# Kernel optimization log

Hardware: AMD Instinct MI355X
Metric: run time of the kernel (lower is better)

The kernel has to match this reference:

```python
import jax, jax.numpy as jnp
import numpy as np

N, E, B = 8192, 131072, 256
F_ATOM, D, H, HD, L, FC, BINS = 92, 256, 8, 32, 6, 512, 256
VMIN, VMAX = 0.0, 8.0


def layer_norm(x, g, b, eps=1e-5):
    mu = jnp.mean(x, axis=-1, keepdims=True)
    var = jnp.var(x, axis=-1, keepdims=True)
    return (x - mu) * jax.lax.rsqrt(var + eps) * g + b


def silu(x):
    return x * jax.nn.sigmoid(x)


def setup_inputs() -> dict:
    key = jax.random.key(0)
    ks = iter(jax.random.split(key, 80))

    def lin(fan_in, shape):
        return jax.random.normal(next(ks), shape, jnp.float32) / np.sqrt(fan_in)

    inp = {
        'x': jax.random.normal(next(ks), (N, F_ATOM), jnp.float32),
        'edge_attr': jax.random.normal(next(ks), (E, 3), jnp.float32) * 2.0,
        'edge_index': jax.random.randint(next(ks), (2, E), 0, N, dtype=jnp.int32),
        'batch': jnp.sort(jax.random.randint(next(ks), (N,), 0, B, dtype=jnp.int32)),
        # atom_embedding: Linear(92,256) -> LN -> SiLU -> Linear(256,256)
        'aw1': lin(F_ATOM, (F_ATOM, D)), 'ab1': jnp.zeros((D,)),
        'ag1': jnp.ones((D,)), 'abt1': jnp.zeros((D,)),
        'aw2': lin(D, (D, D)), 'ab2': jnp.zeros((D,)),
        # rbf MLP: Linear(256,256) LN SiLU Linear LN SiLU Linear
        'rw1': lin(BINS, (BINS, D)), 'rb1': jnp.zeros((D,)),
        'rg1': jnp.ones((D,)), 'rbt1': jnp.zeros((D,)),
        'rw2': lin(D, (D, D)), 'rb2': jnp.zeros((D,)),
        'rg2': jnp.ones((D,)), 'rbt2': jnp.zeros((D,)),
        'rw3': lin(D, (D, D)), 'rb3': jnp.zeros((D,)),
        # L stacked PrdnetConv (edge-conditioned multi-head graph attention)
        'Wq': lin(D, (L, D, D)), 'bq': jnp.zeros((L, D)),
        'Wk': lin(D, (L, D, D)), 'bk': jnp.zeros((L, D)),
        'Wv': lin(D, (L, D, D)), 'bv': jnp.zeros((L, D)),
        'We': lin(D, (L, D, D)), 'be': jnp.zeros((L, D)),
        'Wo': lin(D, (L, D, D)), 'bo': jnp.zeros((L, D)),
        'lng': jnp.ones((L, D)), 'lnb': jnp.zeros((L, D)),
        # FC head: Linear(256,512) then fc_out Linear(512,1)
        'fw1': lin(D, (D, FC)), 'fb1': jnp.zeros((FC,)),
        'fow': lin(FC, (FC, 1)), 'fob': jnp.zeros((1,)),
    }
    return inp


def _forward(x, edge_attr, edge_index, batch, aw1, ab1, ag1, abt1, aw2, ab2,
             rw1, rb1, rg1, rbt1, rw2, rb2, rg2, rbt2, rw3, rb3,
             Wq, bq, Wk, bk, Wv, bv, We, be, Wo, bo, lng, lnb,
             fw1, fb1, fow, fob):
    # atom embedding (dropout = identity at inference)
    node = silu(layer_norm(x @ aw1 + ab1, ag1, abt1)) @ aw2 + ab2  # [N, D]

    # RBF expansion of edge lengths, then edge MLP
    d = jnp.linalg.norm(edge_attr, axis=1)  # [E]
    centers = jnp.linspace(VMIN, VMAX, BINS)
    gamma = 1.0 / (centers[1] - centers[0]) ** 2
    rbf = jnp.exp(-gamma * (d[:, None] - centers[None, :]) ** 2)  # [E, BINS]
    e = silu(layer_norm(rbf @ rw1 + rb1, rg1, rbt1))
    e = silu(layer_norm(e @ rw2 + rb2, rg2, rbt2))
    e = e @ rw3 + rb3  # [E, D]

    src, dst = edge_index[0], edge_index[1]
    inv_sqrt = 1.0 / np.sqrt(HD)
    for l in range(L):
        res = node
        q = (node @ Wq[l] + bq[l]).reshape(N, H, HD)
        k = (node @ Wk[l] + bk[l]).reshape(N, H, HD)
        v = (node @ Wv[l] + bv[l]).reshape(N, H, HD)
        ee = (e @ We[l] + be[l]).reshape(E, H, HD)
        kj = k[src] + ee  # edge-conditioned keys [E, H, HD]
        vj = v[src] + ee  # edge-conditioned values
        score = jnp.sum(q[dst] * kj, axis=-1) * inv_sqrt  # [E, H]
        smax = jax.ops.segment_max(score, dst, num_segments=N)  # [N, H]
        ex = jnp.exp(score - smax[dst])
        den = jax.ops.segment_sum(ex, dst, num_segments=N)
        alpha = ex / (den[dst] + 1e-16)  # neighborhood softmax [E, H]
        msg = jax.ops.segment_sum(alpha[:, :, None] * vj, dst, num_segments=N)
        out = msg.reshape(N, D) @ Wo[l] + bo[l]
        out = layer_norm(out, lng[l], lnb[l])
        node = out + res  # residual

    # scatter-mean graph pooling
    sums = jax.ops.segment_sum(node, batch, num_segments=B)  # [B, D]
    cnt = jax.ops.segment_sum(jnp.ones((N,), node.dtype), batch, num_segments=B)
    feats = sums / jnp.clip(cnt, 1.0)[:, None]

    feats = feats @ fw1 + fb1  # single fc layer: no act (i == len-1 in source)
    return feats @ fow + fob  # [B, 1], identity link


def reference(x, edge_attr, edge_index, batch, aw1, ab1, ag1, abt1, aw2, ab2,
              rw1, rb1, rg1, rbt1, rw2, rb2, rg2, rbt2, rw3, rb3,
              Wq, bq, Wk, bk, Wv, bv, We, be, Wo, bo, lng, lnb,
              fw1, fb1, fow, fob):
    return _forward(x, edge_attr, edge_index, batch, aw1, ab1, ag1, abt1, aw2,
                    ab2, rw1, rb1, rg1, rbt1, rw2, rb2, rg2, rbt2, rw3, rb3,
                    Wq, bq, Wk, bk, Wv, bv, We, be, Wo, bo, lng, lnb,
                    fw1, fb1, fow, fob)
```

## Files before the change

kernel.cpp:

```cpp
#include <hip/hip_runtime.h>
#include <hip/hip_bf16.h>
#include <cstddef>

#define NN    8192
#define EE    131072
#define BB    256
#define F_AT  92
#define DD    256
#define HH    8
#define HDIM  32
#define LL    6
#define FCD   512

typedef __hip_bfloat16 bf16;
typedef __attribute__((ext_vector_type(8))) __bf16 bf16x8;
typedef __attribute__((ext_vector_type(4))) float f32x4;

__device__ __forceinline__ float to_f(float x) { return x; }
__device__ __forceinline__ float to_f(bf16 x) { return __bfloat162float(x); }
__device__ __forceinline__ float bfu(unsigned short u) {
    return __uint_as_float(((unsigned)u) << 16);
}
__device__ __forceinline__ unsigned short bfbits(float x) {
    bf16 h = __float2bfloat16(x);
    return *(unsigned short*)&h;
}
__device__ __forceinline__ void store_v(float* p, float v) { *p = v; }
__device__ __forceinline__ void store_v(bf16* p, float v) { *p = __float2bfloat16(v); }

__device__ __forceinline__ float4 load4(const float* p) { return *(const float4*)p; }
__device__ __forceinline__ float4 load4(const bf16* p) {
    const ushort4 r = *(const ushort4*)p;
    return make_float4(bfu(r.x), bfu(r.y), bfu(r.z), bfu(r.w));
}

__device__ __forceinline__ void store_f4(float* p, const float4& f) {
    *(float4*)p = f;
}
__device__ __forceinline__ void store_f4(bf16* p, const float4& f) {
    ushort4 u = {bfbits(f.x), bfbits(f.y), bfbits(f.z), bfbits(f.w)};
    *(ushort4*)p = u;
}

__device__ __forceinline__ bf16x8 ld8(const bf16* p) { return *(const bf16x8*)p; }
__device__ __forceinline__ bf16x8 ld8(const float* p) {
    const float4 f0 = *(const float4*)p;
    const float4 f1 = *(const float4*)(p + 4);
    bf16x8 r;
    r[0] = (__bf16)f0.x; r[1] = (__bf16)f0.y; r[2] = (__bf16)f0.z; r[3] = (__bf16)f0.w;
    r[4] = (__bf16)f1.x; r[5] = (__bf16)f1.y; r[6] = (__bf16)f1.z; r[7] = (__bf16)f1.w;
    return r;
}

__device__ __forceinline__ void async_copy16(const void* g, void* l) {
    __builtin_amdgcn_global_load_lds(
        (const __attribute__((address_space(1))) unsigned int*)g,
        (__attribute__((address_space(3))) unsigned int*)l, 16, 0, 0);
}

__global__ __launch_bounds__(256) void transpose_weights(
    const float* __restrict__ rw1, const float* __restrict__ rw2,
    const float* __restrict__ rw3, const float* __restrict__ aw2,
    const float* __restrict__ Wq, const float* __restrict__ Wk,
    const float* __restrict__ Wv, const float* __restrict__ We,
    const float* __restrict__ Wo, __bf16* __restrict__ out)
{
    __shared__ float tile[64][65];
    const int midx = blockIdx.y;
    const float* src;
    if (midx == 0) src = rw1;
    else if (midx == 1) src = rw2;
    else if (midx == 2) src = rw3;
    else if (midx == 3) src = aw2;
    else {
        const int l = (midx - 4) / 5, s = (midx - 4) % 5;
        const float* bases[5] = {Wq, Wk, Wv, We, Wo};
        src = bases[s] + (size_t)l * 65536;
    }
    __bf16* dst = out + (size_t)midx * 65536;
    const int k0 = (blockIdx.x >> 2) * 64;
    const int n0 = (blockIdx.x & 3) * 64;
    const int c = threadIdx.x & 63;
    const int r0 = threadIdx.x >> 6;
#pragma unroll
    for (int p = 0; p < 16; ++p) {
        const int r = r0 + p * 4;
        tile[r][c] = src[(size_t)(k0 + r) * 256 + n0 + c];
    }
    __syncthreads();
#pragma unroll
    for (int p = 0; p < 16; ++p) {
        const int n = r0 + p * 4;
        dst[(size_t)(n0 + n) * 256 + k0 + c] = (__bf16)tile[c][n];
    }
}

__global__ __launch_bounds__(256) void pack_qkv_bias(
    const float* __restrict__ bq, const float* __restrict__ bk,
    const float* __restrict__ bv, float* __restrict__ out)
{
    const int i = blockIdx.x * 256 + threadIdx.x;
    if (i >= LL * 768) return;
    const int l = i / 768, r = i % 768;
    const float* s = (r < 256) ? bq : (r < 512) ? bk : bv;
    out[i] = s[l * 256 + (r & 255)];
}

__global__ __launch_bounds__(256) void combine_w3e(
    const float* __restrict__ rw3, const float* __restrict__ We,
    __bf16* __restrict__ Wt_out)
{
    __shared__ float As[16][65];
    __shared__ float Ws[16][65];
    const int l = blockIdx.z;
    const float* W = We + (size_t)l * 65536;
    __bf16* dst = Wt_out + (size_t)l * 65536;
    const int m0 = blockIdx.x * 64;
    const int n0 = blockIdx.y * 64;
    const int tid = threadIdx.x;
    const int tx = tid & 15, ty = tid >> 4;
    float acc[4][4] = {};

    for (int k0 = 0; k0 < 256; k0 += 16) {
        {
            const int ar = tid >> 2;
            const int ac = (tid & 3) * 4;
#pragma unroll
            for (int j = 0; j < 4; ++j)
                As[ac + j][ar] = rw3[(size_t)(m0 + ar) * 256 + k0 + ac + j];
        }
        {
            const int wr = tid >> 4;
            const int wc = (tid & 15) * 4;
#pragma unroll
            for (int j = 0; j < 4; ++j)
                Ws[wr][wc + j] = W[(size_t)(k0 + wr) * 256 + n0 + wc + j];
        }
        __syncthreads();
#pragma unroll
        for (int kk = 0; kk < 16; ++kk) {
            float a[4], b[4];
#pragma unroll
            for (int i = 0; i < 4; ++i) a[i] = As[kk][ty * 4 + i];
#pragma unroll
            for (int j = 0; j < 4; ++j) b[j] = Ws[kk][tx * 4 + j];
#pragma unroll
            for (int i = 0; i < 4; ++i)
#pragma unroll
                for (int j = 0; j < 4; ++j) acc[i][j] += a[i] * b[j];
        }
        __syncthreads();
    }
#pragma unroll
    for (int i = 0; i < 4; ++i) {
        const int gk = m0 + ty * 4 + i;
#pragma unroll
        for (int j = 0; j < 4; ++j) {
            const int gn = n0 + tx * 4 + j;
            dst[(size_t)gn * 256 + gk] = (__bf16)acc[i][j];
        }
    }
}

__global__ __launch_bounds__(256) void combine_bias(
    const float* __restrict__ rb3, const float* __restrict__ We,
    const float* __restrict__ be, float* __restrict__ out)
{
    const int l = blockIdx.x;
    const int n = threadIdx.x;
    const float* W = We + (size_t)l * 65536;
    float s = be[l * 256 + n];
    for (int m = 0; m < 256; ++m) s += rb3[m] * W[m * 256 + n];
    out[l * 256 + n] = s;
}

__global__ __launch_bounds__(256) void mfma_gemm_ln(
    const bf16* __restrict__ A, const __bf16* __restrict__ Wt,
    const float* __restrict__ bias, const float* __restrict__ g,
    const float* __restrict__ b, bf16* __restrict__ C, int do_silu)
{
    __shared__ __align__(16) __bf16 As[64 * 64];
    __shared__ __align__(16) __bf16 Bs[256 * 64];
    const int tid = threadIdx.x;
    const int m0 = blockIdx.x * 64;
    const int wave = tid >> 6, lane = tid & 63;
    const int lm = lane & 15, lq = lane >> 4;
    const int lrow = lane >> 3;
    const int lcolsw = ((lane & 7) ^ lrow) * 8;

    f32x4 acc[16] = {};

    for (int k0 = 0; k0 < 256; k0 += 64) {
#pragma unroll
        for (int p = 0; p < 2; ++p) {
            const int rbase = wave * 16 + p * 8;
            async_copy16(A + (size_t)(m0 + rbase + lrow) * 256 + k0 + lcolsw,
                         As + rbase * 64);
        }
#pragma unroll
        for (int p = 0; p < 8; ++p) {
            const int rbase = wave * 64 + p * 8;
            async_copy16(Wt + (size_t)(rbase + lrow) * 256 + k0 + lcolsw,
                         Bs + rbase * 64);
        }
        __syncthreads();
#pragma unroll
        for (int ks = 0; ks < 2; ++ks) {
            const int sw = ((ks * 4 + lq) ^ (lm & 7)) * 8;
            const bf16x8 a = *(const bf16x8*)(As + (wave * 16 + lm) * 64 + sw);
#pragma unroll
            for (int j = 0; j < 16; ++j) {
                const bf16x8 bf = *(const bf16x8*)(Bs + (j * 16 + lm) * 64 + sw);
                acc[j] = __builtin_amdgcn_mfma_f32_16x16x32_bf16(a, bf, acc[j], 0, 0, 0);
            }
        }
        __syncthreads();
    }

    float gg[16], bb[16];
#pragma unroll
    for (int j = 0; j < 16; ++j) {
        const float bv = bias[j * 16 + lm];
        gg[j] = g[j * 16 + lm];
        bb[j] = b[j * 16 + lm];
#pragma unroll
        for (int r = 0; r < 4; ++r) acc[j][r] += bv;
    }

#pragma unroll
    for (int r = 0; r < 4; ++r) {
        float s = 0.f, q = 0.f;
#pragma unroll
        for (int j = 0; j < 16; ++j) { const float v = acc[j][r]; s += v; q += v * v; }
#pragma unroll
        for (int msk = 1; msk < 16; msk <<= 1) {
            s += __shfl_xor(s, msk);
            q += __shfl_xor(q, msk);
        }
        const float mean = s * (1.f / 256.f);
        const float var = q * (1.f / 256.f) - mean * mean;
        const float rs = rsqrtf(var + 1e-5f);
        bf16* crow = C + (size_t)(m0 + wave * 16 + lq * 4 + r) * 256;
#pragma unroll
        for (int j = 0; j < 16; ++j) {
            float v = (acc[j][r] - mean) * rs * gg[j] + bb[j];
            if (do_silu) v = v / (1.f + __expf(-v));
            crow[j * 16 + lm] = __float2bfloat16(v);
        }
    }
}

template <typename CT>
__global__ __launch_bounds__(256) void mfma_gemm_async(
    const bf16* __restrict__ A, const __bf16* __restrict__ Wt,
    const float* __restrict__ bias, CT* __restrict__ C,
    int M, int Nn, int K)
{
    __shared__ __align__(16) __bf16 As[128 * 64];
    __shared__ __align__(16) __bf16 Bs[128 * 64];
    const int tid = threadIdx.x;
    const int m0 = blockIdx.x * 128;
    const int n0 = blockIdx.y * 128;
    const int wave = tid >> 6, lane = tid & 63;
    const int wm = (wave & 1) * 64, wn = (wave >> 1) * 64;
    const int lm = lane & 15, lq = lane >> 4;
    const int lrow = lane >> 3;
    const int lcolsw = ((lane & 7) ^ lrow) * 8;

    f32x4 acc[4][4] = {};

    for (int k0 = 0; k0 < K; k0 += 64) {
#pragma unroll
        for (int p = 0; p < 4; ++p) {
            const int rbase = wave * 32 + p * 8;
            async_copy16(A  + (size_t)(m0 + rbase + lrow) * K + k0 + lcolsw,
                         As + rbase * 64);
            async_copy16(Wt + (size_t)(n0 + rbase + lrow) * K + k0 + lcolsw,
                         Bs + rbase * 64);
        }
        __syncthreads();
#pragma unroll
        for (int ks = 0; ks < 2; ++ks) {
            const int sw = ((ks * 4 + lq) ^ (lm & 7)) * 8;
            bf16x8 a[4], b[4];
#pragma unroll
            for (int i = 0; i < 4; ++i) {
                a[i] = *(const bf16x8*)(As + (wm + i * 16 + lm) * 64 + sw);
                b[i] = *(const bf16x8*)(Bs + (wn + i * 16 + lm) * 64 + sw);
            }
#pragma unroll
            for (int i = 0; i < 4; ++i)
#pragma unroll
                for (int j = 0; j < 4; ++j)
                    acc[i][j] = __builtin_amdgcn_mfma_f32_16x16x32_bf16(
                        a[i], b[j], acc[i][j], 0, 0, 0);
        }
        __syncthreads();
    }

#pragma unroll
    for (int i = 0; i < 4; ++i) {
        const int gm = m0 + wm + i * 16 + lq * 4;
#pragma unroll
        for (int j = 0; j < 4; ++j) {
            const int gn = n0 + wn + j * 16 + lm;
            const float bv = bias ? bias[gn] : 0.f;
#pragma unroll
            for (int r = 0; r < 4; ++r)
                store_v(&C[(size_t)(gm + r) * Nn + gn], acc[i][j][r] + bv);
        }
    }
}

template <typename AT, typename CT>
__global__ __launch_bounds__(256) void mfma_gemm(
    const AT* __restrict__ A, const __bf16* __restrict__ Wt,
    const float* __restrict__ bias, CT* __restrict__ C,
    int M, int Nn, int K)
{
    __shared__ __align__(16) __bf16 As[128 * 72];
    __shared__ __align__(16) __bf16 Bs[128 * 72];
    const int tid = threadIdx.x;
    const int m0 = blockIdx.x * 128;
    const int n0 = blockIdx.y * 128;
    const int wave = tid >> 6, lane = tid & 63;
    const int wm = (wave & 1) * 64, wn = (wave >> 1) * 64;
    const int lm = lane & 15, lq = lane >> 4;

    f32x4 acc[4][4] = {};

    const int srow = tid >> 3;
    const int scol = (tid & 7) * 8;

    for (int k0 = 0; k0 < K; k0 += 64) {
#pragma unroll
        for (int p = 0; p < 4; ++p) {
            const int r = srow + 32 * p;
            *(bf16x8*)(As + r * 72 + scol) = ld8(A + (size_t)(m0 + r) * K + k0 + scol);
            *(bf16x8*)(Bs + r * 72 + scol) = *(const bf16x8*)(Wt + (size_t)(n0 + r) * K + k0 + scol);
        }
        __syncthreads();
#pragma unroll
        for (int ks = 0; ks < 2; ++ks) {
            bf16x8 a[4], b[4];
#pragma unroll
            for (int i = 0; i < 4; ++i) {
                a[i] = *(const bf16x8*)(As + (wm + i * 16 + lm) * 72 + ks * 32 + lq * 8);
                b[i] = *(const bf16x8*)(Bs + (wn + i * 16 + lm) * 72 + ks * 32 + lq * 8);
            }
#pragma unroll
            for (int i = 0; i < 4; ++i)
#pragma unroll
                for (int j = 0; j < 4; ++j)
                    acc[i][j] = __builtin_amdgcn_mfma_f32_16x16x32_bf16(
                        a[i], b[j], acc[i][j], 0, 0, 0);
        }
        __syncthreads();
    }

#pragma unroll
    for (int i = 0; i < 4; ++i) {
        const int gm = m0 + wm + i * 16 + lq * 4;
#pragma unroll
        for (int j = 0; j < 4; ++j) {
            const int gn = n0 + wn + j * 16 + lm;
            const float bv = bias ? bias[gn] : 0.f;
#pragma unroll
            for (int r = 0; r < 4; ++r)
                store_v(&C[(size_t)(gm + r) * Nn + gn], acc[i][j][r] + bv);
        }
    }
}

template <typename AT, typename CT>
__global__ __launch_bounds__(256) void gemm_bias(
    const AT* __restrict__ A, const float* __restrict__ W,
    const float* __restrict__ bias, CT* __restrict__ C,
    int M, int Nn, int K)
{
    __shared__ float As[16][65];
    __shared__ float Ws[16][65];
    const int m0 = blockIdx.x * 64;
    const int n0 = blockIdx.y * 64;
    const int tid = threadIdx.x;
    const int tx = tid & 15, ty = tid >> 4;
    float acc[4][4] = {};

    for (int k0 = 0; k0 < K; k0 += 16) {
        {
            const int ar = tid >> 2;
            const int ac = (tid & 3) * 4;
            const int gm = m0 + ar;
#pragma unroll
            for (int j = 0; j < 4; ++j) {
                const int gk = k0 + ac + j;
                float v = 0.f;
                if (gm < M && gk < K) v = to_f(A[(size_t)gm * K + gk]);
                As[ac + j][ar] = v;
            }
        }
        {
            const int wr = tid >> 4;
            const int wc = (tid & 15) * 4;
            const int gk = k0 + wr;
#pragma unroll
            for (int j = 0; j < 4; ++j) {
                float v = 0.f;
                if (gk < K) v = W[(size_t)gk * Nn + n0 + wc + j];
                Ws[wr][wc + j] = v;
            }
        }
        __syncthreads();
#pragma unroll
        for (int kk = 0; kk < 16; ++kk) {
            float a[4], b[4];
#pragma unroll
            for (int i = 0; i < 4; ++i) a[i] = As[kk][ty * 4 + i];
#pragma unroll
            for (int j = 0; j < 4; ++j) b[j] = Ws[kk][tx * 4 + j];
#pragma unroll
            for (int i = 0; i < 4; ++i)
#pragma unroll
                for (int j = 0; j < 4; ++j) acc[i][j] += a[i] * b[j];
        }
        __syncthreads();
    }
#pragma unroll
    for (int i = 0; i < 4; ++i) {
        const int gm = m0 + ty * 4 + i;
        if (gm >= M) continue;
#pragma unroll
        for (int j = 0; j < 4; ++j) {
            const int gn = n0 + tx * 4 + j;
            float v = acc[i][j];
            if (bias) v += bias[gn];
            store_v(&C[(size_t)gm * Nn + gn], v);
        }
    }
}

__global__ __launch_bounds__(256) void rbf_kernel(
    const float* __restrict__ ea, bf16* __restrict__ rbf)
{
    const int e = blockIdx.x * 4 + (threadIdx.x >> 6);
    const int c0 = (threadIdx.x & 63) * 4;
    const float ax = ea[e * 3 + 0];
    const float ay = ea[e * 3 + 1];
    const float az = ea[e * 3 + 2];
    const float d = sqrtf(ax * ax + ay * ay + az * az);
    const float step = 8.0f / 255.0f;
    const float gamma = 1.0f / (step * step);
    float o[4];
#pragma unroll
    for (int j = 0; j < 4; ++j) {
        const float t = d - (float)(c0 + j) * step;
        o[j] = __expf(-gamma * t * t);
    }
    store_f4(rbf + (size_t)e * DD + c0, make_float4(o[0], o[1], o[2], o[3]));
}

template <typename XT, typename YT>
__global__ __launch_bounds__(256) void ln_act_kernel(
    const XT* __restrict__ X, YT* __restrict__ Y,
    const float* __restrict__ g, const float* __restrict__ b,
    const float* __restrict__ resid, int rows, int do_silu)
{
    const int wave = threadIdx.x >> 6;
    const int lane = threadIdx.x & 63;
    const int r = blockIdx.x * 4 + wave;
    if (r >= rows) return;
    const float4 x = load4(X + (size_t)r * DD + lane * 4);
    float s = x.x + x.y + x.z + x.w;
    float q = x.x * x.x + x.y * x.y + x.z * x.z + x.w * x.w;
    for (int off = 32; off; off >>= 1) {
        s += __shfl_down(s, off);
        q += __shfl_down(q, off);
    }
    s = __shfl(s, 0);
    q = __shfl(q, 0);
    const float mean = s * (1.f / 256.f);
    const float var = q * (1.f / 256.f) - mean * mean;
    const float rs = rsqrtf(var + 1e-5f);
    const int c = lane * 4;
    float xs[4] = {x.x, x.y, x.z, x.w};
    float out[4];
#pragma unroll
    for (int i = 0; i < 4; ++i) {
        float v = (xs[i] - mean) * rs * g[c + i] + b[c + i];
        if (do_silu) v = v / (1.f + __expf(-v));
        out[i] = v;
    }
    if (resid) {
        const float4 rv = load4(resid + (size_t)r * DD + c);
        out[0] += rv.x; out[1] += rv.y; out[2] += rv.z; out[3] += rv.w;
    }
    store_f4(Y + (size_t)r * DD + c, make_float4(out[0], out[1], out[2], out[3]));
}

__global__ __launch_bounds__(256) void deg_kernel(
    const int* __restrict__ dst, int* __restrict__ deg)
{
    const int e = blockIdx.x * 256 + threadIdx.x;
    if (e < EE) atomicAdd(&deg[dst[e]], 1);
}

__global__ __launch_bounds__(256) void csr_scan(
    const int* __restrict__ deg, int* __restrict__ rowptr)
{
    __shared__ int part[256];
    const int t = threadIdx.x;
    int local[32];
    int s = 0;
#pragma unroll
    for (int i = 0; i < 32; ++i) { local[i] = deg[t * 32 + i]; s += local[i]; }
    part[t] = s;
    __syncthreads();
    if (t == 0) {
        int run = 0;
        for (int i = 0; i < 256; ++i) { const int v = part[i]; part[i] = run; run += v; }
    }
    __syncthreads();
    int run = part[t];
#pragma unroll
    for (int i = 0; i < 32; ++i) { rowptr[t * 32 + i] = run; run += local[i]; }
    if (t == 255) rowptr[NN] = run;
}

__global__ __launch_bounds__(256) void fill_kernel(
    const int* __restrict__ dst, const int* __restrict__ rowptr,
    int* __restrict__ fill, int* __restrict__ eid)
{
    const int e = blockIdx.x * 256 + threadIdx.x;
    if (e >= EE) return;
    const int d = dst[e];
    const int pos = atomicAdd(&fill[d], 1);
    eid[rowptr[d] + pos] = e;
}

__global__ __launch_bounds__(256) void attn_kernel(
    const bf16* __restrict__ qkv, const bf16* __restrict__ ee,
    const int* __restrict__ rowptr, const int* __restrict__ eid,
    const int* __restrict__ src, float* __restrict__ msg)
{
    const int n = blockIdx.x;
    const int tid = threadIdx.x;
    const int wave = tid >> 6, lane = tid & 63;
    const int e0 = rowptr[n];
    const int deg = rowptr[n + 1] - e0;

    if (deg == 0) {
        msg[(size_t)n * DD + tid] = 0.f;
        return;
    }

    __shared__ float wm[4][HH];
    __shared__ float wl[4][HH];
    __shared__ float wacc[4][DD];

    const float4 qreg = load4(qkv + (size_t)n * 768 + lane * 4);

    float m = -3.402823466e38f, l = 0.f;
    float4 acc = {0.f, 0.f, 0.f, 0.f};

    for (int j = wave; j < deg; j += 4) {
        const int e = eid[e0 + j];
        const int s_ = src[e];
        const bf16* srow = qkv + (size_t)s_ * 768;
        const float4 kv = load4(srow + 256 + lane * 4);
        const float4 vv = load4(srow + 512 + lane * 4);
        const float4 ev = load4(ee + (size_t)e * DD + lane * 4);
        float p = qreg.x * (kv.x + ev.x) + qreg.y * (kv.y + ev.y) +
                  qreg.z * (kv.z + ev.z) + qreg.w * (kv.w + ev.w);
        p += __shfl_down(p, 4);
        p += __shfl_down(p, 2);
        p += __shfl_down(p, 1);
        const float s = __shfl(p, lane & 56) * 0.17677669529663687f;
        const float mnew = fmaxf(m, s);
        const float scale = __expf(m - mnew);
        const float pe = __expf(s - mnew);
        l = l * scale + pe;
        acc.x = acc.x * scale + pe * (vv.x + ev.x);
        acc.y = acc.y * scale + pe * (vv.y + ev.y);
        acc.z = acc.z * scale + pe * (vv.z + ev.z);
        acc.w = acc.w * scale + pe * (vv.w + ev.w);
        m = mnew;
    }

    if ((lane & 7) == 0) { wm[wave][lane >> 3] = m; wl[wave][lane >> 3] = l; }
    *(float4*)(&wacc[wave][lane * 4]) = acc;
    __syncthreads();

    {
        const int c = tid, h = tid >> 5;
        float M = wm[0][h];
#pragma unroll
        for (int i = 1; i < 4; ++i) M = fmaxf(M, wm[i][h]);
        float L = 0.f, num = 0.f;
#pragma unroll
        for (int i = 0; i < 4; ++i) {
            const float sc = __expf(wm[i][h] - M);
            L += wl[i][h] * sc;
            num += wacc[i][c] * sc;
        }
        msg[(size_t)n * DD + c] = num / (L + 1e-16f);
    }
}

__global__ __launch_bounds__(256) void zero_kernel(float* __restrict__ p, int n)
{
    const int i = blockIdx.x * 256 + threadIdx.x;
    if (i < n) p[i] = 0.f;
}

__global__ __launch_bounds__(256) void pool_kernel(
    const float* __restrict__ node, const int* __restrict__ batch,
    float* __restrict__ sums, float* __restrict__ cnt)
{
    const int n = blockIdx.x;
    const int c = threadIdx.x;
    const int b = batch[n];
    atomicAdd(&sums[b * DD + c], node[(size_t)n * DD + c]);
    if (c == 0) atomicAdd(&cnt[b], 1.0f);
}

__global__ __launch_bounds__(256) void pooled_kernel(
    const float* __restrict__ sums, const float* __restrict__ cnt,
    float* __restrict__ pooled)
{
    const int b = blockIdx.x;
    const int c = threadIdx.x;
    float cc = cnt[b];
    if (cc < 1.f) cc = 1.f;
    pooled[b * DD + c] = sums[b * DD + c] / cc;
}

__global__ __launch_bounds__(64) void final_kernel(
    const float* __restrict__ fc, const float* __restrict__ fow,
    const float* __restrict__ fob, float* __restrict__ out)
{
    const int b = blockIdx.x;
    const int lane = threadIdx.x;
    float s = 0.f;
#pragma unroll
    for (int i = lane; i < FCD; i += 64) s += fc[(size_t)b * FCD + i] * fow[i];
    for (int off = 32; off; off >>= 1) s += __shfl_down(s, off);
    if (lane == 0) out[b] = s + fob[0];
}

extern "C" void kernel_launch(void* const* d_in, const int* in_sizes, int n_in,
                              void* d_out, int out_size, void* d_ws,
                              size_t ws_size, hipStream_t stream)
{
    const float* x         = (const float*)d_in[0];
    const float* edge_attr = (const float*)d_in[1];
    const int*   eidx      = (const int*)d_in[2];
    const int*   batch     = (const int*)d_in[3];
    const float* aw1 = (const float*)d_in[4];
    const float* ab1 = (const float*)d_in[5];
    const float* ag1 = (const float*)d_in[6];
    const float* abt1 = (const float*)d_in[7];
    const float* aw2 = (const float*)d_in[8];
    const float* ab2 = (const float*)d_in[9];
    const float* rw1 = (const float*)d_in[10];
    const float* rb1 = (const float*)d_in[11];
    const float* rg1 = (const float*)d_in[12];
    const float* rbt1 = (const float*)d_in[13];
    const float* rw2 = (const float*)d_in[14];
    const float* rb2 = (const float*)d_in[15];
    const float* rg2 = (const float*)d_in[16];
    const float* rbt2 = (const float*)d_in[17];
    const float* rw3 = (const float*)d_in[18];
    const float* rb3 = (const float*)d_in[19];
    const float* Wq = (const float*)d_in[20];
    const float* bq = (const float*)d_in[21];
    const float* Wk = (const float*)d_in[22];
    const float* bk = (const float*)d_in[23];
    const float* Wv = (const float*)d_in[24];
    const float* bv = (const float*)d_in[25];
    const float* We_ = (const float*)d_in[26];
    const float* be_ = (const float*)d_in[27];
    const float* Wo = (const float*)d_in[28];
    const float* bo = (const float*)d_in[29];
    const float* lng = (const float*)d_in[30];
    const float* lnb = (const float*)d_in[31];
    const float* fw1 = (const float*)d_in[32];
    const float* fb1 = (const float*)d_in[33];
    const float* fow = (const float*)d_in[34];
    const float* fob = (const float*)d_in[35];

    const int* src = eidx;
    const int* dst = eidx + EE;

    char* w = (char*)d_ws;
    size_t off = 0;
    auto alloc = [&](size_t bytes) -> void* {
        void* p = w + off;
        off += (bytes + 255) & ~(size_t)255;
        return p;
    };
    bf16* t_buf = (bf16*)alloc((size_t)EE * DD * 2);
    bf16* e_buf = (bf16*)alloc((size_t)EE * DD * 2);
    float* node = (float*)alloc((size_t)NN * DD * 4);
    bf16*  qkv  = (bf16*)alloc((size_t)NN * 768 * 2);
    float* msg  = (float*)alloc((size_t)NN * DD * 4);
    float* outb = (float*)alloc((size_t)NN * DD * 4);
    int* deg    = (int*)alloc((size_t)NN * 4);
    int* fillc  = (int*)alloc((size_t)NN * 4);
    int* rowptr = (int*)alloc((size_t)(NN + 1) * 4);
    int* eid    = (int*)alloc((size_t)EE * 4);
    float* sums  = (float*)alloc((size_t)BB * DD * 4);
    float* cnt   = (float*)alloc((size_t)BB * 4);
    float* pooled = (float*)alloc((size_t)BB * DD * 4);
    float* fc    = (float*)alloc((size_t)BB * FCD * 4);
    __bf16* Wt  = (__bf16*)alloc((size_t)40 * 65536 * 2);
    float* qkvb = (float*)alloc((size_t)LL * 768 * 4);
    float* be_c = (float*)alloc((size_t)LL * 256 * 4);
    (void)ws_size; (void)n_in; (void)in_sizes; (void)out_size;

    const dim3 blk(256);
    auto WT = [&](int i) -> const __bf16* { return Wt + (size_t)i * 65536; };

    hipLaunchKernelGGL(transpose_weights, dim3(16, 34), blk, 0, stream,
                       rw1, rw2, rw3, aw2, Wq, Wk, Wv, We_, Wo, Wt);
    hipLaunchKernelGGL(combine_w3e, dim3(4, 4, LL), blk, 0, stream, rw3, We_, Wt + (size_t)34 * 65536);
    hipLaunchKernelGGL(combine_bias, dim3(LL), blk, 0, stream, rb3, We_, be_, be_c);
    hipLaunchKernelGGL(pack_qkv_bias, dim3((LL * 768 + 255) / 256), blk, 0, stream, bq, bk, bv, qkvb);
    hipLaunchKernelGGL(zero_kernel, dim3((2 * NN + 255) / 256), blk, 0, stream, (float*)deg, 2 * NN);
    hipLaunchKernelGGL(deg_kernel, dim3(EE / 256), blk, 0, stream, dst, deg);
    hipLaunchKernelGGL(csr_scan, dim3(1), blk, 0, stream, deg, rowptr);
    hipLaunchKernelGGL(fill_kernel, dim3(EE / 256), blk, 0, stream, dst, rowptr, fillc, eid);

    hipLaunchKernelGGL(rbf_kernel, dim3(EE / 4), blk, 0, stream, edge_attr, t_buf);
    hipLaunchKernelGGL(mfma_gemm_ln, dim3(EE / 64), blk, 0, stream, t_buf, WT(0), rb1, rg1, rbt1, e_buf, 1);
    hipLaunchKernelGGL(mfma_gemm_ln, dim3(EE / 64), blk, 0, stream, e_buf, WT(1), rb2, rg2, rbt2, t_buf, 1);

    {
        dim3 gn64(NN / 64, DD / 64);
        hipLaunchKernelGGL((gemm_bias<float, float>), gn64, blk, 0, stream, x, aw1, ab1, outb, NN, DD, F_AT);
        hipLaunchKernelGGL((ln_act_kernel<float, float>), dim3(NN / 4), blk, 0, stream, outb, outb, ag1, abt1, (const float*)nullptr, NN, 1);
        hipLaunchKernelGGL((mfma_gemm<float, float>), dim3(NN / 128, DD / 128), blk, 0, stream, outb, WT(3), ab2, node, NN, DD, DD);
    }

    const dim3 geM(EE / 128, DD / 128);
    for (int l = 0; l < LL; ++l) {
        const size_t bo_ = (size_t)l * DD;
        hipLaunchKernelGGL((mfma_gemm<float, bf16>), dim3(NN / 128, 768 / 128), blk, 0, stream,
                           node, WT(4 + 5 * l), qkvb + (size_t)l * 768, qkv, NN, 768, DD);
        hipLaunchKernelGGL((mfma_gemm_async<bf16>), geM, blk, 0, stream, t_buf, WT(34 + l), be_c + (size_t)l * 256, e_buf, EE, DD, DD);
        hipLaunchKernelGGL(attn_kernel, dim3(NN), blk, 0, stream, qkv, e_buf, rowptr, eid, src, msg);
        hipLaunchKernelGGL((mfma_gemm<float, float>), dim3(NN / 128, DD / 128), blk, 0, stream, msg, WT(8 + 5 * l), bo + bo_, outb, NN, DD, DD);
        hipLaunchKernelGGL((ln_act_kernel<float, float>), dim3(NN / 4), blk, 0, stream, outb, node, lng + bo_, lnb + bo_, node, NN, 0);
    }

    const int PZ = BB * DD + BB;
    hipLaunchKernelGGL(zero_kernel, dim3((PZ + 255) / 256), blk, 0, stream, sums, PZ);
    hipLaunchKernelGGL(pool_kernel, dim3(NN), blk, 0, stream, node, batch, sums, cnt);
    hipLaunchKernelGGL(pooled_kernel, dim3(BB), blk, 0, stream, sums, cnt, pooled);
    {
        dim3 gf(BB / 64, FCD / 64);
        hipLaunchKernelGGL((gemm_bias<float, float>), gf, blk, 0, stream, pooled, fw1, fb1, fc, BB, FCD, DD);
    }
    hipLaunchKernelGGL(final_kernel, dim3(BB), dim3(64), 0, stream, fc, fow, fob, (float*)d_out);
}
```

Baseline: 1.043 ms.

## Reorder edge features into CSR order and batch edge projections across layers

```diff
diff --git a/kernel.cpp b/kernel.cpp
--- a/kernel.cpp
+++ b/kernel.cpp
@@ -440,9 +440,11 @@
 }
 
 __global__ __launch_bounds__(256) void rbf_kernel(
-    const float* __restrict__ ea, bf16* __restrict__ rbf)
-{
-    const int e = blockIdx.x * 4 + (threadIdx.x >> 6);
+    const float* __restrict__ ea, const int* __restrict__ eid,
+    bf16* __restrict__ rbf)
+{
+    const int p = blockIdx.x * 4 + (threadIdx.x >> 6);
+    const int e = eid[p];
     const int c0 = (threadIdx.x & 63) * 4;
     const float ax = ea[e * 3 + 0];
     const float ay = ea[e * 3 + 1];
@@ -456,7 +458,7 @@
         const float t = d - (float)(c0 + j) * step;
         o[j] = __expf(-gamma * t * t);
     }
-    store_f4(rbf + (size_t)e * DD + c0, make_float4(o[0], o[1], o[2], o[3]));
+    store_f4(rbf + (size_t)p * DD + c0, make_float4(o[0], o[1], o[2], o[3]));
 }
 
 template <typename XT, typename YT>
@@ -527,20 +529,23 @@
 }
 
 __global__ __launch_bounds__(256) void fill_kernel(
-    const int* __restrict__ dst, const int* __restrict__ rowptr,
-    int* __restrict__ fill, int* __restrict__ eid)
+    const int* __restrict__ src, const int* __restrict__ dst,
+    const int* __restrict__ rowptr, int* __restrict__ fill,
+    int* __restrict__ eid, int* __restrict__ srcc)
 {
     const int e = blockIdx.x * 256 + threadIdx.x;
     if (e >= EE) return;
     const int d = dst[e];
     const int pos = atomicAdd(&fill[d], 1);
-    eid[rowptr[d] + pos] = e;
+    const int q = rowptr[d] + pos;
+    eid[q] = e;
+    srcc[q] = src[e];
 }
 
 __global__ __launch_bounds__(256) void attn_kernel(
-    const bf16* __restrict__ qkv, const bf16* __restrict__ ee,
-    const int* __restrict__ rowptr, const int* __restrict__ eid,
-    const int* __restrict__ src, float* __restrict__ msg)
+    const bf16* __restrict__ qkv, const bf16* __restrict__ ee, int estride,
+    const int* __restrict__ rowptr, const int* __restrict__ srcc,
+    float* __restrict__ msg)
 {
     const int n = blockIdx.x;
     const int tid = threadIdx.x;
@@ -563,12 +568,12 @@
     float4 acc = {0.f, 0.f, 0.f, 0.f};
 
     for (int j = wave; j < deg; j += 4) {
-        const int e = eid[e0 + j];
-        const int s_ = src[e];
+        const int e = e0 + j;
+        const int s_ = srcc[e];
         const bf16* srow = qkv + (size_t)s_ * 768;
         const float4 kv = load4(srow + 256 + lane * 4);
         const float4 vv = load4(srow + 512 + lane * 4);
-        const float4 ev = load4(ee + (size_t)e * DD + lane * 4);
+        const float4 ev = load4(ee + (size_t)e * estride + lane * 4);
         float p = qreg.x * (kv.x + ev.x) + qreg.y * (kv.y + ev.y) +
                   qreg.z * (kv.z + ev.z) + qreg.w * (kv.w + ev.w);
         p += __shfl_down(p, 4);
@@ -699,7 +704,6 @@
         return p;
     };
     bf16* t_buf = (bf16*)alloc((size_t)EE * DD * 2);
-    bf16* e_buf = (bf16*)alloc((size_t)EE * DD * 2);
     float* node = (float*)alloc((size_t)NN * DD * 4);
     bf16*  qkv  = (bf16*)alloc((size_t)NN * 768 * 2);
     float* msg  = (float*)alloc((size_t)NN * DD * 4);
@@ -708,6 +712,7 @@
     int* fillc  = (int*)alloc((size_t)NN * 4);
     int* rowptr = (int*)alloc((size_t)(NN + 1) * 4);
     int* eid    = (int*)alloc((size_t)EE * 4);
+    int* srcc   = (int*)alloc((size_t)EE * 4);
     float* sums  = (float*)alloc((size_t)BB * DD * 4);
     float* cnt   = (float*)alloc((size_t)BB * 4);
     float* pooled = (float*)alloc((size_t)BB * DD * 4);
@@ -715,7 +720,14 @@
     __bf16* Wt  = (__bf16*)alloc((size_t)40 * 65536 * 2);
     float* qkvb = (float*)alloc((size_t)LL * 768 * 4);
     float* be_c = (float*)alloc((size_t)LL * 256 * 4);
-    (void)ws_size; (void)n_in; (void)in_sizes; (void)out_size;
+
+    const size_t avail = (off <= ws_size) ? ws_size - off : 0;
+    int G = 1;
+    if      (avail >= (size_t)EE * (6 * DD) * 2 + 256) G = 6;
+    else if (avail >= (size_t)EE * (3 * DD) * 2 + 256) G = 3;
+    else if (avail >= (size_t)EE * (2 * DD) * 2 + 256) G = 2;
+    bf16* e_slab = (bf16*)alloc((size_t)EE * (G * DD) * 2);
+    (void)n_in; (void)in_sizes; (void)out_size;
 
     const dim3 blk(256);
     auto WT = [&](int i) -> const __bf16* { return Wt + (size_t)i * 65536; };
@@ -728,11 +740,11 @@
     hipLaunchKernelGGL(zero_kernel, dim3((2 * NN + 255) / 256), blk, 0, stream, (float*)deg, 2 * NN);
     hipLaunchKernelGGL(deg_kernel, dim3(EE / 256), blk, 0, stream, dst, deg);
     hipLaunchKernelGGL(csr_scan, dim3(1), blk, 0, stream, deg, rowptr);
-    hipLaunchKernelGGL(fill_kernel, dim3(EE / 256), blk, 0, stream, dst, rowptr, fillc, eid);
-
-    hipLaunchKernelGGL(rbf_kernel, dim3(EE / 4), blk, 0, stream, edge_attr, t_buf);
-    hipLaunchKernelGGL(mfma_gemm_ln, dim3(EE / 64), blk, 0, stream, t_buf, WT(0), rb1, rg1, rbt1, e_buf, 1);
-    hipLaunchKernelGGL(mfma_gemm_ln, dim3(EE / 64), blk, 0, stream, e_buf, WT(1), rb2, rg2, rbt2, t_buf, 1);
+    hipLaunchKernelGGL(fill_kernel, dim3(EE / 256), blk, 0, stream, src, dst, rowptr, fillc, eid, srcc);
+
+    hipLaunchKernelGGL(rbf_kernel, dim3(EE / 4), blk, 0, stream, edge_attr, eid, t_buf);
+    hipLaunchKernelGGL(mfma_gemm_ln, dim3(EE / 64), blk, 0, stream, t_buf, WT(0), rb1, rg1, rbt1, e_slab, 1);
+    hipLaunchKernelGGL(mfma_gemm_ln, dim3(EE / 64), blk, 0, stream, e_slab, WT(1), rb2, rg2, rbt2, t_buf, 1);
 
     {
         dim3 gn64(NN / 64, DD / 64);
@@ -741,13 +753,16 @@
         hipLaunchKernelGGL((mfma_gemm<float, float>), dim3(NN / 128, DD / 128), blk, 0, stream, outb, WT(3), ab2, node, NN, DD, DD);
     }
 
-    const dim3 geM(EE / 128, DD / 128);
     for (int l = 0; l < LL; ++l) {
         const size_t bo_ = (size_t)l * DD;
         hipLaunchKernelGGL((mfma_gemm<float, bf16>), dim3(NN / 128, 768 / 128), blk, 0, stream,
                            node, WT(4 + 5 * l), qkvb + (size_t)l * 768, qkv, NN, 768, DD);
-        hipLaunchKernelGGL((mfma_gemm_async<bf16>), geM, blk, 0, stream, t_buf, WT(34 + l), be_c + (size_t)l * 256, e_buf, EE, DD, DD);
-        hipLaunchKernelGGL(attn_kernel, dim3(NN), blk, 0, stream, qkv, e_buf, rowptr, eid, src, msg);
+        if (l % G == 0) {
+            hipLaunchKernelGGL((mfma_gemm_async<bf16>), dim3(EE / 128, (G * DD) / 128), blk, 0, stream,
+                               t_buf, WT(34 + l), be_c + (size_t)l * 256, e_slab, EE, G * DD, DD);
+        }
+        const bf16* ee_l = e_slab + (size_t)(l % G) * DD;
+        hipLaunchKernelGGL(attn_kernel, dim3(NN), blk, 0, stream, qkv, ee_l, G * DD, rowptr, srcc, msg);
         hipLaunchKernelGGL((mfma_gemm<float, float>), dim3(NN / 128, DD / 128), blk, 0, stream, msg, WT(8 + 5 * l), bo + bo_, outb, NN, DD, DD);
         hipLaunchKernelGGL((ln_act_kernel<float, float>), dim3(NN / 4), blk, 0, stream, outb, node, lng + bo_, lnb + bo_, node, NN, 0);
     }
```

Measured after the change: 1.034 ms. No clear change (-0.8%).
